# Optimization experiments

Hardware: AMD Instinct MI355X
Metric: run time of the kernel (lower is better)

Reference implementation:

```python
import jax, jax.numpy as jnp
import numpy as np
from jax.ops import segment_sum

N_NODES = 50000


def graph_conv(src, dst, x, W, b, n_nodes):
    # DGL GraphConv with norm='both' (allow_zero_in_degree=True):
    # h = D_in^{-1/2} * A^T (D_out^{-1/2} * x) W + b, degrees clamped to >=1
    ones = jnp.ones(src.shape[0], dtype=x.dtype)
    deg_out = jnp.clip(segment_sum(ones, src, num_segments=n_nodes), 1.0)
    deg_in = jnp.clip(segment_sum(ones, dst, num_segments=n_nodes), 1.0)
    h = x * jax.lax.rsqrt(deg_out)[:, None]
    h = h @ W                      # apply weight before aggregation (mult_W first)
    m = segment_sum(h[src], dst, num_segments=n_nodes)  # sparse neighbor sum
    return m * jax.lax.rsqrt(deg_in)[:, None] + b


def setup_inputs() -> dict:
    key = jax.random.key(0)
    ks = jax.random.split(key, 10)
    n, e = N_NODES, 1600000
    d_in, h1, h2, h3 = 128, 128, 128, 64
    in_feat = jax.random.normal(ks[0], (n, d_in), dtype=jnp.float32)
    src = jax.random.randint(ks[1], (e,), 0, n, dtype=jnp.int32)
    dst = jax.random.randint(ks[2], (e,), 0, n, dtype=jnp.int32)
    s = lambda fi, fo: (1.0 / np.sqrt(fi)).astype(np.float32)
    W1 = jax.random.normal(ks[3], (d_in, h1), dtype=jnp.float32) * s(d_in, h1)
    b1 = jnp.zeros((h1,), dtype=jnp.float32)
    W2 = jax.random.normal(ks[4], (h1, h2), dtype=jnp.float32) * s(h1, h2)
    b2 = jnp.zeros((h2,), dtype=jnp.float32)
    Wf = jax.random.normal(ks[5], (h2, h3), dtype=jnp.float32) * s(h2, h3)
    bf = jnp.zeros((h3,), dtype=jnp.float32)
    return {"in_feat": in_feat, "src": src, "dst": dst,
            "W1": W1, "b1": b1, "W2": W2, "b2": b2, "Wf": Wf, "bf": bf}


def reference(in_feat, src, dst, W1, b1, W2, b2, Wf, bf):
    n = in_feat.shape[0]
    h = graph_conv(src, dst, in_feat, W1, b1, n)
    h = jax.nn.relu(h)
    # dropout(p=0.2) is identity in eval mode
    h = graph_conv(src, dst, h, W2, b2, n)
    return h @ Wf + bf
```

## Files before the change

kernel.cpp:

```cpp
#include <hip/hip_runtime.h>
#include <hip/hip_fp16.h>

#define FD 128
#define OD 64
#define RN 256
#define CHUNKS 256
#define NRMAX 1024

typedef _Float16 f16x8 __attribute__((ext_vector_type(8)));
typedef float    f32x4 __attribute__((ext_vector_type(4)));


__global__ void prescale_kernel(const float* __restrict__ X, const float* __restrict__ r_out,
                                __half* __restrict__ Xs, int n4) {
    int i = blockIdx.x * 256 + threadIdx.x;
    if (i >= n4) return;
    int v = i >> 5;
    float r = r_out[v];
    float4 t = ((const float4*)X)[i];
    __half2 h0 = __floats2half2_rn(t.x * r, t.y * r);
    __half2 h1 = __floats2half2_rn(t.z * r, t.w * r);
    ((__half2*)Xs)[2 * i]     = h0;
    ((__half2*)Xs)[2 * i + 1] = h1;
}


__global__ __launch_bounds__(1024) void region_hist_kernel(const int* __restrict__ src,
                                                           const int* __restrict__ dst,
                                                           int* __restrict__ hist_g,
                                                           int* __restrict__ hist_gs,
                                                           int E, int NR, int CS) {
    __shared__ int hist[NRMAX];
    __shared__ int hist_s[NRMAX];
    int c = blockIdx.x;
    for (int t = threadIdx.x; t < NR; t += 1024) { hist[t] = 0; hist_s[t] = 0; }
    __syncthreads();
    int e0 = c * CS, e1 = min(e0 + CS, E);
    int nv = (e1 - e0) & ~3;
    for (int e = e0 + threadIdx.x * 4; e < e0 + nv; e += 4096) {
        int4 d = *(const int4*)(dst + e);
        int4 s = *(const int4*)(src + e);
        atomicAdd(&hist[d.x >> 8], 1);
        atomicAdd(&hist[d.y >> 8], 1);
        atomicAdd(&hist[d.z >> 8], 1);
        atomicAdd(&hist[d.w >> 8], 1);
        atomicAdd(&hist_s[s.x >> 8], 1);
        atomicAdd(&hist_s[s.y >> 8], 1);
        atomicAdd(&hist_s[s.z >> 8], 1);
        atomicAdd(&hist_s[s.w >> 8], 1);
    }
    for (int e = e0 + nv + threadIdx.x; e < e1; e += 1024) {
        atomicAdd(&hist[dst[e] >> 8], 1);
        atomicAdd(&hist_s[src[e] >> 8], 1);
    }
    __syncthreads();
    for (int t = threadIdx.x; t < NR; t += 1024) {
        hist_g[c * NR + t]  = hist[t];
        hist_gs[c * NR + t] = hist_s[t];
    }
}

__global__ __launch_bounds__(1024) void region_scan_kernel(const int* __restrict__ hist_g,
                                                           const int* __restrict__ hist_gs,
                                                           int* __restrict__ rstart,
                                                           int* __restrict__ cursor,
                                                           int* __restrict__ sstart,
                                                           int* __restrict__ scursor,
                                                           int NR, int E) {
    __shared__ int wsum[16];
    int tid = threadIdx.x, lane = tid & 63, w = tid >> 6;
    int total = 0;
    if (tid < NR)
        for (int c = 0; c < CHUNKS; c++) total += hist_g[c * NR + tid];
    int x = total;
    #pragma unroll
    for (int d = 1; d < 64; d <<= 1) {
        int t = __shfl_up(x, d, 64);
        if (lane >= d) x += t;
    }
    if (lane == 63) wsum[w] = x;
    __syncthreads();
    if (w == 0) {
        int s = (lane < 16) ? wsum[lane] : 0;
        #pragma unroll
        for (int d = 1; d < 16; d <<= 1) {
            int t = __shfl_up(s, d, 64);
            if (lane >= d) s += t;
        }
        if (lane < 16) wsum[lane] = s;
    }
    __syncthreads();
    int off = (w == 0) ? 0 : wsum[w - 1];
    if (tid < NR) {
        int start = x + off - total;
        rstart[tid] = start;
        int run = start;
        for (int c = 0; c < CHUNKS; c++) {
            cursor[c * NR + tid] = run;
            run += hist_g[c * NR + tid];
        }
    }
    if (tid == 0) rstart[NR] = E;
    __syncthreads();
    total = 0;
    if (tid < NR)
        for (int c = 0; c < CHUNKS; c++) total += hist_gs[c * NR + tid];
    x = total;
    #pragma unroll
    for (int d = 1; d < 64; d <<= 1) {
        int t = __shfl_up(x, d, 64);
        if (lane >= d) x += t;
    }
    if (lane == 63) wsum[w] = x;
    __syncthreads();
    if (w == 0) {
        int s = (lane < 16) ? wsum[lane] : 0;
        #pragma unroll
        for (int d = 1; d < 16; d <<= 1) {
            int t = __shfl_up(s, d, 64);
            if (lane >= d) s += t;
        }
        if (lane < 16) wsum[lane] = s;
    }
    __syncthreads();
    off = (w == 0) ? 0 : wsum[w - 1];
    if (tid < NR) {
        int start = x + off - total;
        sstart[tid] = start;
        int run = start;
        for (int c = 0; c < CHUNKS; c++) {
            scursor[c * NR + tid] = run;
            run += hist_gs[c * NR + tid];
        }
    }
    if (tid == 0) sstart[NR] = E;
}

__global__ __launch_bounds__(1024) void partition_kernel(const int* __restrict__ src,
                                                         const int* __restrict__ dst,
                                                         const int* __restrict__ cursor,
                                                         const int* __restrict__ scursor,
                                                         int* __restrict__ epack,
                                                         unsigned char* __restrict__ spack,
                                                         int E, int NR, int CS) {
    __shared__ int cur[NRMAX];
    __shared__ int scur[NRMAX];
    int c = blockIdx.x;
    for (int t = threadIdx.x; t < NR; t += 1024) {
        cur[t]  = cursor[c * NR + t];
        scur[t] = scursor[c * NR + t];
    }
    __syncthreads();
    int e0 = c * CS, e1 = min(e0 + CS, E);
    int nv = (e1 - e0) & ~3;
    for (int e = e0 + threadIdx.x * 4; e < e0 + nv; e += 4096) {
        int4 d = *(const int4*)(dst + e);
        int4 s = *(const int4*)(src + e);
        int p0 = atomicAdd(&cur[d.x >> 8], 1);
        int p1 = atomicAdd(&cur[d.y >> 8], 1);
        int p2 = atomicAdd(&cur[d.z >> 8], 1);
        int p3 = atomicAdd(&cur[d.w >> 8], 1);
        epack[p0] = ((d.x & 255) << 17) | s.x;
        epack[p1] = ((d.y & 255) << 17) | s.y;
        epack[p2] = ((d.z & 255) << 17) | s.z;
        epack[p3] = ((d.w & 255) << 17) | s.w;
        int q0 = atomicAdd(&scur[s.x >> 8], 1);
        int q1 = atomicAdd(&scur[s.y >> 8], 1);
        int q2 = atomicAdd(&scur[s.z >> 8], 1);
        int q3 = atomicAdd(&scur[s.w >> 8], 1);
        spack[q0] = (unsigned char)(s.x & 255);
        spack[q1] = (unsigned char)(s.y & 255);
        spack[q2] = (unsigned char)(s.z & 255);
        spack[q3] = (unsigned char)(s.w & 255);
    }
    for (int e = e0 + nv + threadIdx.x; e < e1; e += 1024) {
        int d = dst[e], s = src[e];
        int pos = atomicAdd(&cur[d >> 8], 1);
        epack[pos] = ((d & 255) << 17) | s;
        int qos = atomicAdd(&scur[s >> 8], 1);
        spack[qos] = (unsigned char)(s & 255);
    }
}

__global__ __launch_bounds__(1024) void region_sort_kernel(const int* __restrict__ epack,
                                                           const int* __restrict__ rstart,
                                                           int* __restrict__ csrc,
                                                           int* __restrict__ row_start,
                                                           float* __restrict__ r_in,
                                                           int N, int NR, int E) {
    __shared__ int cnt[RN];
    __shared__ int cur[RN];
    __shared__ int wsum[16];
    const int r = blockIdx.x, tid = threadIdx.x;
    const int lane = tid & 63, w = tid >> 6;
    const int s0 = rstart[r], s1 = rstart[r + 1];
    if (tid < RN) cnt[tid] = 0;
    __syncthreads();
    for (int e = s0 + tid; e < s1; e += 1024)
        atomicAdd(&cnt[epack[e] >> 17], 1);
    __syncthreads();
    int cv = (tid < RN) ? cnt[tid] : 0;
    int x = cv;
    #pragma unroll
    for (int d = 1; d < 64; d <<= 1) {
        int t = __shfl_up(x, d, 64);
        if (lane >= d) x += t;
    }
    if (lane == 63 && w < 4) wsum[w] = x;
    __syncthreads();
    if (tid < RN) {
        int woff = 0;
        for (int i = 0; i < w; i++) woff += wsum[i];
        int start = s0 + x - cv + woff;
        cur[tid] = start;
        int node = r * RN + tid;
        if (node < N) {
            row_start[node] = start;
            r_in[node] = rsqrtf((float)max(cv, 1));
        }
    }
    if (r == NR - 1 && tid == 0) row_start[N] = E;
    __syncthreads();
    for (int e = s0 + tid; e < s1; e += 1024) {
        int pk = epack[e];
        int pos = atomicAdd(&cur[pk >> 17], 1);
        csrc[pos] = pk & 0x1FFFF;
    }
}

__global__ __launch_bounds__(256) void rout2_kernel(const unsigned char* __restrict__ spack,
                                                    const int* __restrict__ sstart,
                                                    float* __restrict__ r_out, int N) {
    __shared__ int cnt[RN];
    const int r = blockIdx.x, tid = threadIdx.x;
    const int s0 = sstart[r], s1 = sstart[r + 1];
    cnt[tid] = 0;
    __syncthreads();
    for (int e = s0 + tid; e < s1; e += 256)
        atomicAdd(&cnt[spack[e]], 1);
    __syncthreads();
    int node = r * RN + tid;
    if (node < N) r_out[node] = rsqrtf((float)max(cnt[tid], 1));
}

__global__ __launch_bounds__(256) void agg128_kernel(const __half* __restrict__ Xs,
                                                     const float* __restrict__ r_in,
                                                     const int* __restrict__ rs,
                                                     const int* __restrict__ csrc,
                                                     __half* __restrict__ Z, int N) {
    const int lane = threadIdx.x & 63, wv = threadIdx.x >> 6;
    int v = blockIdx.x * 4 + wv;
    if (v >= N) return;
    int s0 = rs[v], s1 = rs[v + 1];
    float ax = 0.f, ay = 0.f;
    int e = s0;
    for (; e + 16 <= s1; e += 16) {
        int idx[16];
        #pragma unroll
        for (int u = 0; u < 16; u++) idx[u] = csrc[e + u];
        __half2 t[16];
        #pragma unroll
        for (int u = 0; u < 16; u++)
            t[u] = ((const __half2*)(Xs + (size_t)idx[u] * FD))[lane];
        #pragma unroll
        for (int u = 0; u < 16; u++) {
            float2 f = __half22float2(t[u]);
            ax += f.x; ay += f.y;
        }
    }
    for (; e + 4 <= s1; e += 4) {
        int idx[4];
        #pragma unroll
        for (int u = 0; u < 4; u++) idx[u] = csrc[e + u];
        __half2 t[4];
        #pragma unroll
        for (int u = 0; u < 4; u++)
            t[u] = ((const __half2*)(Xs + (size_t)idx[u] * FD))[lane];
        #pragma unroll
        for (int u = 0; u < 4; u++) {
            float2 f = __half22float2(t[u]);
            ax += f.x; ay += f.y;
        }
    }
    for (; e < s1; e++) {
        float2 f = __half22float2(((const __half2*)(Xs + (size_t)csrc[e] * FD))[lane]);
        ax += f.x; ay += f.y;
    }
    float ri = r_in[v];
    ((__half2*)(Z + (size_t)v * FD))[lane] = __floats2half2_rn(ax * ri, ay * ri);
}

__global__ __launch_bounds__(256) void agg64_kernel(const __half* __restrict__ T,
                                                    const float* __restrict__ r_in,
                                                    const int* __restrict__ rs,
                                                    const int* __restrict__ csrc,
                                                    const float* __restrict__ bc,
                                                    float* __restrict__ out, int N) {
    const int tid = threadIdx.x;
    const int lane = tid & 63, wv = tid >> 6;
    const int hf = lane >> 5, l32 = lane & 31;
    int v = blockIdx.x * 8 + wv * 2 + hf;
    if (v >= N) return;
    int s0 = rs[v], s1 = rs[v + 1];
    float ax = 0.f, ay = 0.f;
    int e = s0;
    for (; e + 8 <= s1; e += 8) {
        int idx[8];
        #pragma unroll
        for (int u = 0; u < 8; u++) idx[u] = csrc[e + u];
        __half2 t[8];
        #pragma unroll
        for (int u = 0; u < 8; u++)
            t[u] = ((const __half2*)(T + (size_t)idx[u] * OD))[l32];
        #pragma unroll
        for (int u = 0; u < 8; u++) {
            float2 f = __half22float2(t[u]);
            ax += f.x; ay += f.y;
        }
    }
    for (; e < s1; e++) {
        float2 f = __half22float2(((const __half2*)(T + (size_t)csrc[e] * OD))[l32]);
        ax += f.x; ay += f.y;
    }
    float ri = r_in[v];
    float2 o;
    o.x = ax * ri + bc[l32 * 2];
    o.y = ay * ri + bc[l32 * 2 + 1];
    ((float2*)(out + (size_t)v * OD))[l32] = o;
}

__global__ __launch_bounds__(256) void gemm1_mfma_kernel(const __half* __restrict__ Ah,
                                                         const __half* __restrict__ Bh,
                                                         const float* __restrict__ b1,
                                                         const float* __restrict__ rowscale,
                                                         __half* __restrict__ Ch,
                                                         int M, int ntiles) {
    const int w = threadIdx.x >> 6, lane = threadIdx.x & 63;
    const int l15 = lane & 15, quad = lane >> 4;
    const _Float16* B = (const _Float16*)Bh;

    f16x8 bfrag[2][4];
    #pragma unroll
    for (int nt = 0; nt < 2; nt++) {
        int col = 32 * w + 16 * nt + l15;
        #pragma unroll
        for (int kk = 0; kk < 4; kk++) {
            int kb = kk * 32 + quad * 8;
            f16x8 bf;
            #pragma unroll
            for (int j = 0; j < 8; j++) bf[j] = B[(size_t)(kb + j) * FD + col];
            bfrag[nt][kk] = bf;
        }
    }

    for (int t = blockIdx.x; t < ntiles; t += gridDim.x) {
        int row0 = t * 16;
        const _Float16* Arow = (const _Float16*)Ah + (size_t)(row0 + l15) * FD + quad * 8;
        f16x8 afrag[4];
        #pragma unroll
        for (int kk = 0; kk < 4; kk++) afrag[kk] = *(const f16x8*)(Arow + kk * 32);
        f32x4 acc0 = {0.f, 0.f, 0.f, 0.f};
        f32x4 acc1 = {0.f, 0.f, 0.f, 0.f};
        #pragma unroll
        for (int kk = 0; kk < 4; kk++) {
            acc0 = __builtin_amdgcn_mfma_f32_16x16x32_f16(afrag[kk], bfrag[0][kk], acc0, 0, 0, 0);
            acc1 = __builtin_amdgcn_mfma_f32_16x16x32_f16(afrag[kk], bfrag[1][kk], acc1, 0, 0, 0);
        }
        int c0 = 32 * w + l15, c1 = c0 + 16;
        float bb0 = b1[c0], bb1 = b1[c1];
        #pragma unroll
        for (int r = 0; r < 4; r++) {
            int row = row0 + quad * 4 + r;
            if (row < M) {
                float rsc = rowscale[row];
                Ch[(size_t)row * FD + c0] = __float2half(fmaxf(acc0[r] + bb0, 0.f) * rsc);
                Ch[(size_t)row * FD + c1] = __float2half(fmaxf(acc1[r] + bb1, 0.f) * rsc);
            }
        }
    }
}

__global__ __launch_bounds__(256) void gemm2_mfma_kernel(const __half* __restrict__ Ah,
                                                         const __half* __restrict__ Bh,
                                                         __half* __restrict__ Ch,
                                                         int M, int ntiles) {
    const int w = threadIdx.x >> 6, lane = threadIdx.x & 63;
    const int l15 = lane & 15, quad = lane >> 4;
    const _Float16* B = (const _Float16*)Bh;

    f16x8 bfrag[4];
    int col = 16 * w + l15;
    #pragma unroll
    for (int kk = 0; kk < 4; kk++) {
        int kb = kk * 32 + quad * 8;
        f16x8 bf;
        #pragma unroll
        for (int j = 0; j < 8; j++) bf[j] = B[(size_t)(kb + j) * OD + col];
        bfrag[kk] = bf;
    }

    for (int t = blockIdx.x; t < ntiles; t += gridDim.x) {
        int row0 = t * 16;
        const _Float16* Arow = (const _Float16*)Ah + (size_t)(row0 + l15) * FD + quad * 8;
        f16x8 afrag[4];
        #pragma unroll
        for (int kk = 0; kk < 4; kk++) afrag[kk] = *(const f16x8*)(Arow + kk * 32);
        f32x4 acc = {0.f, 0.f, 0.f, 0.f};
        #pragma unroll
        for (int kk = 0; kk < 4; kk++)
            acc = __builtin_amdgcn_mfma_f32_16x16x32_f16(afrag[kk], bfrag[kk], acc, 0, 0, 0);
        #pragma unroll
        for (int r = 0; r < 4; r++) {
            int row = row0 + quad * 4 + r;
            if (row < M)
                Ch[(size_t)row * OD + col] = __float2half(acc[r]);
        }
    }
}

__global__ void fold_kernel(const float* __restrict__ W2, const float* __restrict__ Wf,
                            const float* __restrict__ b2, const float* __restrict__ bf,
                            const float* __restrict__ W1,
                            __half* __restrict__ W1h, __half* __restrict__ Wch,
                            float* __restrict__ bc) {
    int idx = blockIdx.x * 256 + threadIdx.x;
    if (idx < FD * FD) W1h[idx] = __float2half(W1[idx]);
    if (idx < FD * OD) {
        int i = idx / OD, j = idx % OD;
        float s = 0.f;
        for (int k = 0; k < FD; k++) s += W2[i * FD + k] * Wf[k * OD + j];
        Wch[idx] = __float2half(s);
    }
    if (idx < OD) {
        float s = bf[idx];
        for (int k = 0; k < FD; k++) s += b2[k] * Wf[k * OD + idx];
        bc[idx] = s;
    }
}

extern "C" void kernel_launch(void* const* d_in, const int* in_sizes, int n_in,
                              void* d_out, int out_size, void* d_ws, size_t ws_size,
                              hipStream_t stream) {
    const float* in_feat = (const float*)d_in[0];
    const int*   src     = (const int*)d_in[1];
    const int*   dst     = (const int*)d_in[2];
    const float* W1      = (const float*)d_in[3];
    const float* b1      = (const float*)d_in[4];
    const float* W2      = (const float*)d_in[5];
    const float* b2      = (const float*)d_in[6];
    const float* Wf      = (const float*)d_in[7];
    const float* bf      = (const float*)d_in[8];
    float* out = (float*)d_out;

    const int N = in_sizes[0] / FD;
    const int E = in_sizes[1];
    const int NR = (N + RN - 1) / RN;
    const int CS = (((E + CHUNKS - 1) / CHUNKS) + 3) & ~3;

    char* ws = (char*)d_ws;
    size_t off = 0;
    auto alloc = [&](size_t bytes) -> void* {
        void* p = ws + off;
        off += (bytes + 255) / 256 * 256;
        return p;
    };
    unsigned char* spack = (unsigned char*)alloc((size_t)E);
    int*    epack   = (int*)alloc((size_t)E * 4);
    __half* tbuf    = (__half*)spack;
    float*  r_out   = (float*)alloc((size_t)N * 4);
    float*  r_in    = (float*)alloc((size_t)N * 4);
    int*    hist_g  = (int*)alloc((size_t)CHUNKS * NR * 4);
    int*    hist_gs = (int*)alloc((size_t)CHUNKS * NR * 4);
    int*    cursor  = (int*)alloc((size_t)CHUNKS * NR * 4);
    int*    scursor = (int*)alloc((size_t)CHUNKS * NR * 4);
    int*    rstart  = (int*)alloc((size_t)(NR + 1) * 4);
    int*    sstart  = (int*)alloc((size_t)(NR + 1) * 4);
    int*    csrc    = (int*)alloc((size_t)E * 4);
    int*    row_start = (int*)alloc((size_t)(N + 1) * 4);
    __half* z1h     = (__half*)alloc((size_t)N * FD * 2);
    __half* y1h     = (__half*)alloc((size_t)N * FD * 2);
    __half* Xs      = (__half*)alloc((size_t)N * FD * 2);
    __half* W1h     = (__half*)alloc((size_t)FD * FD * 2);
    __half* Wch     = (__half*)alloc((size_t)FD * OD * 2);
    float*  bc      = (float*)alloc((size_t)OD * 4);
    (void)ws_size; (void)n_in; (void)out_size;

    const int ntiles = (N + 15) / 16;
    const int gemmgrid = ntiles < 1024 ? ntiles : 1024;

    region_hist_kernel<<<CHUNKS, 1024, 0, stream>>>(src, dst, hist_g, hist_gs, E, NR, CS);
    region_scan_kernel<<<1, 1024, 0, stream>>>(hist_g, hist_gs, rstart, cursor, sstart, scursor, NR, E);
    partition_kernel<<<CHUNKS, 1024, 0, stream>>>(src, dst, cursor, scursor, epack, spack, E, NR, CS);
    region_sort_kernel<<<NR, 1024, 0, stream>>>(epack, rstart, csrc, row_start, r_in, N, NR, E);
    rout2_kernel<<<NR, 256, 0, stream>>>(spack, sstart, r_out, N);

    fold_kernel<<<(FD * FD + 255) / 256, 256, 0, stream>>>(W2, Wf, b2, bf, W1, W1h, Wch, bc);

    prescale_kernel<<<(N * 32 + 255) / 256, 256, 0, stream>>>(in_feat, r_out, Xs, N * 32);
    agg128_kernel<<<(N + 3) / 4, 256, 0, stream>>>(Xs, r_in, row_start, csrc, z1h, N);

    gemm1_mfma_kernel<<<gemmgrid, 256, 0, stream>>>(z1h, W1h, b1, r_out, y1h, N, ntiles);
    gemm2_mfma_kernel<<<gemmgrid, 256, 0, stream>>>(y1h, Wch, tbuf, N, ntiles);

    agg64_kernel<<<(N + 7) / 8, 256, 0, stream>>>(tbuf, r_in, row_start, csrc, bc, out, N);
}
```

Before: 282.3 us.

## Chunk feature dimension into 32-wide slabs for cache-resident neighbor gathers

Stores the prescaled features, the aggregated features and the second-layer transform in a feature-chunked layout: 32 halfs (64 bytes) per node per chunk. Aggregation then runs once per chunk, so each pass gathers from a much smaller table that can stay in L2. Each wave handles one node, with its four 16-lane quads taking different edges, and the partial sums are combined with shuffles. Both GEMMs are adapted to read and write the chunked layout. The cost is reading the edge index list several times, extra kernel launches, and vector index loads that may not be aligned.

After: 390.0 us. 38.1% more time.

```diff
diff --git a/kernel.cpp b/kernel.cpp
--- a/kernel.cpp
+++ b/kernel.cpp
@@ -6,22 +6,27 @@
 #define RN 256
 #define CHUNKS 256
 #define NRMAX 1024
+#define FC 32
 
 typedef _Float16 f16x8 __attribute__((ext_vector_type(8)));
 typedef float    f32x4 __attribute__((ext_vector_type(4)));
 
 
 __global__ void prescale_kernel(const float* __restrict__ X, const float* __restrict__ r_out,
-                                __half* __restrict__ Xs, int n4) {
+                                __half* __restrict__ Xs, int n4, int N) {
     int i = blockIdx.x * 256 + threadIdx.x;
     if (i >= n4) return;
     int v = i >> 5;
+    int fq = i & 31;
     float r = r_out[v];
     float4 t = ((const float4*)X)[i];
     __half2 h0 = __floats2half2_rn(t.x * r, t.y * r);
     __half2 h1 = __floats2half2_rn(t.z * r, t.w * r);
-    ((__half2*)Xs)[2 * i]     = h0;
-    ((__half2*)Xs)[2 * i + 1] = h1;
+    int c  = fq >> 3;
+    int w0 = (fq & 7) * 4;
+    __half2* p = (__half2*)(Xs + ((size_t)c * N + v) * FC + w0);
+    p[0] = h0;
+    p[1] = h1;
 }
 
 
@@ -243,90 +248,108 @@
     if (node < N) r_out[node] = rsqrtf((float)max(cnt[tid], 1));
 }
 
-__global__ __launch_bounds__(256) void agg128_kernel(const __half* __restrict__ Xs,
+__global__ __launch_bounds__(256) void agg32h_kernel(const __half* __restrict__ T,
                                                      const float* __restrict__ r_in,
                                                      const int* __restrict__ rs,
                                                      const int* __restrict__ csrc,
                                                      __half* __restrict__ Z, int N) {
     const int lane = threadIdx.x & 63, wv = threadIdx.x >> 6;
+    const int quad = lane >> 4, l15 = lane & 15;
     int v = blockIdx.x * 4 + wv;
     if (v >= N) return;
-    int s0 = rs[v], s1 = rs[v + 1];
+    int s0 = __builtin_amdgcn_readfirstlane(rs[v]);
+    int s1 = __builtin_amdgcn_readfirstlane(rs[v + 1]);
     float ax = 0.f, ay = 0.f;
     int e = s0;
-    for (; e + 16 <= s1; e += 16) {
-        int idx[16];
-        #pragma unroll
-        for (int u = 0; u < 16; u++) idx[u] = csrc[e + u];
-        __half2 t[16];
-        #pragma unroll
-        for (int u = 0; u < 16; u++)
-            t[u] = ((const __half2*)(Xs + (size_t)idx[u] * FD))[lane];
-        #pragma unroll
-        for (int u = 0; u < 16; u++) {
-            float2 f = __half22float2(t[u]);
-            ax += f.x; ay += f.y;
-        }
-    }
-    for (; e + 4 <= s1; e += 4) {
-        int idx[4];
-        #pragma unroll
-        for (int u = 0; u < 4; u++) idx[u] = csrc[e + u];
-        __half2 t[4];
-        #pragma unroll
-        for (int u = 0; u < 4; u++)
-            t[u] = ((const __half2*)(Xs + (size_t)idx[u] * FD))[lane];
-        #pragma unroll
-        for (int u = 0; u < 4; u++) {
-            float2 f = __half22float2(t[u]);
-            ax += f.x; ay += f.y;
-        }
-    }
-    for (; e < s1; e++) {
-        float2 f = __half22float2(((const __half2*)(Xs + (size_t)csrc[e] * FD))[lane]);
-        ax += f.x; ay += f.y;
-    }
-    float ri = r_in[v];
-    ((__half2*)(Z + (size_t)v * FD))[lane] = __floats2half2_rn(ax * ri, ay * ri);
-}
-
-__global__ __launch_bounds__(256) void agg64_kernel(const __half* __restrict__ T,
-                                                    const float* __restrict__ r_in,
-                                                    const int* __restrict__ rs,
-                                                    const int* __restrict__ csrc,
-                                                    const float* __restrict__ bc,
-                                                    float* __restrict__ out, int N) {
-    const int tid = threadIdx.x;
-    const int lane = tid & 63, wv = tid >> 6;
-    const int hf = lane >> 5, l32 = lane & 31;
-    int v = blockIdx.x * 8 + wv * 2 + hf;
-    if (v >= N) return;
-    int s0 = rs[v], s1 = rs[v + 1];
-    float ax = 0.f, ay = 0.f;
-    int e = s0;
-    for (; e + 8 <= s1; e += 8) {
+    for (; e + 32 <= s1; e += 32) {
         int idx[8];
         #pragma unroll
-        for (int u = 0; u < 8; u++) idx[u] = csrc[e + u];
+        for (int u = 0; u < 8; u++) {
+            int4 q4 = *(const int4*)(csrc + e + 4 * u);
+            idx[u] = quad == 0 ? q4.x : quad == 1 ? q4.y : quad == 2 ? q4.z : q4.w;
+        }
         __half2 t[8];
         #pragma unroll
         for (int u = 0; u < 8; u++)
-            t[u] = ((const __half2*)(T + (size_t)idx[u] * OD))[l32];
+            t[u] = ((const __half2*)(T + (size_t)idx[u] * FC))[l15];
         #pragma unroll
         for (int u = 0; u < 8; u++) {
             float2 f = __half22float2(t[u]);
             ax += f.x; ay += f.y;
         }
     }
+    for (; e + 4 <= s1; e += 4) {
+        int4 q4 = *(const int4*)(csrc + e);
+        int idx = quad == 0 ? q4.x : quad == 1 ? q4.y : quad == 2 ? q4.z : q4.w;
+        float2 f = __half22float2(((const __half2*)(T + (size_t)idx * FC))[l15]);
+        ax += f.x; ay += f.y;
+    }
     for (; e < s1; e++) {
-        float2 f = __half22float2(((const __half2*)(T + (size_t)csrc[e] * OD))[l32]);
+        if (quad == 0) {
+            float2 f = __half22float2(((const __half2*)(T + (size_t)csrc[e] * FC))[l15]);
+            ax += f.x; ay += f.y;
+        }
+    }
+    ax += __shfl_xor(ax, 16); ay += __shfl_xor(ay, 16);
+    ax += __shfl_xor(ax, 32); ay += __shfl_xor(ay, 32);
+    if (quad == 0) {
+        float ri = r_in[v];
+        ((__half2*)(Z + (size_t)v * FC))[l15] = __floats2half2_rn(ax * ri, ay * ri);
+    }
+}
+
+__global__ __launch_bounds__(256) void agg32f_kernel(const __half* __restrict__ T,
+                                                     const float* __restrict__ r_in,
+                                                     const int* __restrict__ rs,
+                                                     const int* __restrict__ csrc,
+                                                     const float* __restrict__ bcc,
+                                                     float* __restrict__ outc, int N) {
+    const int lane = threadIdx.x & 63, wv = threadIdx.x >> 6;
+    const int quad = lane >> 4, l15 = lane & 15;
+    int v = blockIdx.x * 4 + wv;
+    if (v >= N) return;
+    int s0 = __builtin_amdgcn_readfirstlane(rs[v]);
+    int s1 = __builtin_amdgcn_readfirstlane(rs[v + 1]);
+    float ax = 0.f, ay = 0.f;
+    int e = s0;
+    for (; e + 32 <= s1; e += 32) {
+        int idx[8];
+        #pragma unroll
+        for (int u = 0; u < 8; u++) {
+            int4 q4 = *(const int4*)(csrc + e + 4 * u);
+            idx[u] = quad == 0 ? q4.x : quad == 1 ? q4.y : quad == 2 ? q4.z : q4.w;
+        }
+        __half2 t[8];
+        #pragma unroll
+        for (int u = 0; u < 8; u++)
+            t[u] = ((const __half2*)(T + (size_t)idx[u] * FC))[l15];
+        #pragma unroll
+        for (int u = 0; u < 8; u++) {
+            float2 f = __half22float2(t[u]);
+            ax += f.x; ay += f.y;
+        }
+    }
+    for (; e + 4 <= s1; e += 4) {
+        int4 q4 = *(const int4*)(csrc + e);
+        int idx = quad == 0 ? q4.x : quad == 1 ? q4.y : quad == 2 ? q4.z : q4.w;
+        float2 f = __half22float2(((const __half2*)(T + (size_t)idx * FC))[l15]);
         ax += f.x; ay += f.y;
     }
-    float ri = r_in[v];
-    float2 o;
-    o.x = ax * ri + bc[l32 * 2];
-    o.y = ay * ri + bc[l32 * 2 + 1];
-    ((float2*)(out + (size_t)v * OD))[l32] = o;
+    for (; e < s1; e++) {
+        if (quad == 0) {
+            float2 f = __half22float2(((const __half2*)(T + (size_t)csrc[e] * FC))[l15]);
+            ax += f.x; ay += f.y;
+        }
+    }
+    ax += __shfl_xor(ax, 16); ay += __shfl_xor(ay, 16);
+    ax += __shfl_xor(ax, 32); ay += __shfl_xor(ay, 32);
+    if (quad == 0) {
+        float ri = r_in[v];
+        float2 o;
+        o.x = ax * ri + bcc[2 * l15];
+        o.y = ay * ri + bcc[2 * l15 + 1];
+        ((float2*)(outc + (size_t)v * OD))[l15] = o;
+    }
 }
 
 __global__ __launch_bounds__(256) void gemm1_mfma_kernel(const __half* __restrict__ Ah,
@@ -338,6 +361,7 @@
     const int w = threadIdx.x >> 6, lane = threadIdx.x & 63;
     const int l15 = lane & 15, quad = lane >> 4;
     const _Float16* B = (const _Float16*)Bh;
+    const _Float16* Az = (const _Float16*)Ah;
 
     f16x8 bfrag[2][4];
     #pragma unroll
@@ -355,10 +379,10 @@
 
     for (int t = blockIdx.x; t < ntiles; t += gridDim.x) {
         int row0 = t * 16;
-        const _Float16* Arow = (const _Float16*)Ah + (size_t)(row0 + l15) * FD + quad * 8;
         f16x8 afrag[4];
         #pragma unroll
-        for (int kk = 0; kk < 4; kk++) afrag[kk] = *(const f16x8*)(Arow + kk * 32);
+        for (int kk = 0; kk < 4; kk++)
+            afrag[kk] = *(const f16x8*)(Az + ((size_t)kk * M + row0 + l15) * FC + quad * 8);
         f32x4 acc0 = {0.f, 0.f, 0.f, 0.f};
         f32x4 acc1 = {0.f, 0.f, 0.f, 0.f};
         #pragma unroll
@@ -390,6 +414,7 @@
 
     f16x8 bfrag[4];
     int col = 16 * w + l15;
+    const int cc = col >> 5, cw = col & 31;
     #pragma unroll
     for (int kk = 0; kk < 4; kk++) {
         int kb = kk * 32 + quad * 8;
@@ -413,7 +438,7 @@
         for (int r = 0; r < 4; r++) {
             int row = row0 + quad * 4 + r;
             if (row < M)
-                Ch[(size_t)row * OD + col] = __float2half(acc[r]);
+                Ch[((size_t)cc * M + row) * FC + cw] = __float2half(acc[r]);
         }
     }
 }
@@ -496,11 +521,15 @@
 
     fold_kernel<<<(FD * FD + 255) / 256, 256, 0, stream>>>(W2, Wf, b2, bf, W1, W1h, Wch, bc);
 
-    prescale_kernel<<<(N * 32 + 255) / 256, 256, 0, stream>>>(in_feat, r_out, Xs, N * 32);
-    agg128_kernel<<<(N + 3) / 4, 256, 0, stream>>>(Xs, r_in, row_start, csrc, z1h, N);
+    prescale_kernel<<<(N * 32 + 255) / 256, 256, 0, stream>>>(in_feat, r_out, Xs, N * 32, N);
+    for (int c = 0; c < 4; c++)
+        agg32h_kernel<<<(N + 3) / 4, 256, 0, stream>>>(Xs + (size_t)c * N * FC, r_in, row_start,
+                                                       csrc, z1h + (size_t)c * N * FC, N);
 
     gemm1_mfma_kernel<<<gemmgrid, 256, 0, stream>>>(z1h, W1h, b1, r_out, y1h, N, ntiles);
     gemm2_mfma_kernel<<<gemmgrid, 256, 0, stream>>>(y1h, Wch, tbuf, N, ntiles);
 
-    agg64_kernel<<<(N + 7) / 8, 256, 0, stream>>>(tbuf, r_in, row_start, csrc, bc, out, N);
-}
+    for (int c = 0; c < 2; c++)
+        agg32f_kernel<<<(N + 3) / 4, 256, 0, stream>>>(tbuf + (size_t)c * N * FC, r_in, row_start,
+                                                       csrc, bc + c * FC, out + c * FC, N);
+}
```

## Transpose histogram layout and software-pipeline index loads in aggregation kernels

Applied to the files above, without the earlier changes.

The per-chunk region histograms and cursors are stored region-major instead of chunk-major. This lets the single-block scan kernel read and write each region's 256 counts with int4 vector accesses instead of strided scalar ones. The gather-aggregation kernels now prefetch the next block of edge indices while the current block's feature rows are loaded, and replace the scalar tail loops with one masked, clamped batch. They also use nontemporal loads and stores for indices and outputs. The cost is more complex code, some wasted loads in the tail, and larger workspace allocations sized by NRMAX.

After: 287.0 us. Within noise of the previous version (+1.7%).

```diff
diff --git a/kernel.cpp b/kernel.cpp
--- a/kernel.cpp
+++ b/kernel.cpp
@@ -9,6 +9,7 @@
 
 typedef _Float16 f16x8 __attribute__((ext_vector_type(8)));
 typedef float    f32x4 __attribute__((ext_vector_type(4)));
+typedef float    f32x2 __attribute__((ext_vector_type(2)));
 
 
 __global__ void prescale_kernel(const float* __restrict__ X, const float* __restrict__ r_out,
@@ -18,10 +19,8 @@
     int v = i >> 5;
     float r = r_out[v];
     float4 t = ((const float4*)X)[i];
-    __half2 h0 = __floats2half2_rn(t.x * r, t.y * r);
-    __half2 h1 = __floats2half2_rn(t.z * r, t.w * r);
-    ((__half2*)Xs)[2 * i]     = h0;
-    ((__half2*)Xs)[2 * i + 1] = h1;
+    ((__half2*)Xs)[2 * i]     = __floats2half2_rn(t.x * r, t.y * r);
+    ((__half2*)Xs)[2 * i + 1] = __floats2half2_rn(t.z * r, t.w * r);
 }
 
 
@@ -55,8 +54,8 @@
     }
     __syncthreads();
     for (int t = threadIdx.x; t < NR; t += 1024) {
-        hist_g[c * NR + t]  = hist[t];
-        hist_gs[c * NR + t] = hist_s[t];
+        hist_g[t * CHUNKS + c]  = hist[t];
+        hist_gs[t * CHUNKS + c] = hist_s[t];
     }
 }
 
@@ -70,8 +69,14 @@
     __shared__ int wsum[16];
     int tid = threadIdx.x, lane = tid & 63, w = tid >> 6;
     int total = 0;
-    if (tid < NR)
-        for (int c = 0; c < CHUNKS; c++) total += hist_g[c * NR + tid];
+    if (tid < NR) {
+        const int4* hp = (const int4*)(hist_g + (size_t)tid * CHUNKS);
+        #pragma unroll 8
+        for (int c4 = 0; c4 < CHUNKS / 4; c4++) {
+            int4 h = hp[c4];
+            total += h.x + h.y + h.z + h.w;
+        }
+    }
     int x = total;
     #pragma unroll
     for (int d = 1; d < 64; d <<= 1) {
@@ -95,16 +100,30 @@
         int start = x + off - total;
         rstart[tid] = start;
         int run = start;
-        for (int c = 0; c < CHUNKS; c++) {
-            cursor[c * NR + tid] = run;
-            run += hist_g[c * NR + tid];
+        const int4* hp = (const int4*)(hist_g + (size_t)tid * CHUNKS);
+        int4* cp = (int4*)(cursor + (size_t)tid * CHUNKS);
+        #pragma unroll 8
+        for (int c4 = 0; c4 < CHUNKS / 4; c4++) {
+            int4 h = hp[c4];
+            int4 o;
+            o.x = run; run += h.x;
+            o.y = run; run += h.y;
+            o.z = run; run += h.z;
+            o.w = run; run += h.w;
+            cp[c4] = o;
         }
     }
     if (tid == 0) rstart[NR] = E;
     __syncthreads();
     total = 0;
-    if (tid < NR)
-        for (int c = 0; c < CHUNKS; c++) total += hist_gs[c * NR + tid];
+    if (tid < NR) {
+        const int4* hp = (const int4*)(hist_gs + (size_t)tid * CHUNKS);
+        #pragma unroll 8
+        for (int c4 = 0; c4 < CHUNKS / 4; c4++) {
+            int4 h = hp[c4];
+            total += h.x + h.y + h.z + h.w;
+        }
+    }
     x = total;
     #pragma unroll
     for (int d = 1; d < 64; d <<= 1) {
@@ -128,9 +147,17 @@
         int start = x + off - total;
         sstart[tid] = start;
         int run = start;
-        for (int c = 0; c < CHUNKS; c++) {
-            scursor[c * NR + tid] = run;
-            run += hist_gs[c * NR + tid];
+        const int4* hp = (const int4*)(hist_gs + (size_t)tid * CHUNKS);
+        int4* cp = (int4*)(scursor + (size_t)tid * CHUNKS);
+        #pragma unroll 8
+        for (int c4 = 0; c4 < CHUNKS / 4; c4++) {
+            int4 h = hp[c4];
+            int4 o;
+            o.x = run; run += h.x;
+            o.y = run; run += h.y;
+            o.z = run; run += h.z;
+            o.w = run; run += h.w;
+            cp[c4] = o;
         }
     }
     if (tid == 0) sstart[NR] = E;
@@ -147,8 +174,8 @@
     __shared__ int scur[NRMAX];
     int c = blockIdx.x;
     for (int t = threadIdx.x; t < NR; t += 1024) {
-        cur[t]  = cursor[c * NR + t];
-        scur[t] = scursor[c * NR + t];
+        cur[t]  = cursor[(size_t)t * CHUNKS + c];
+        scur[t] = scursor[(size_t)t * CHUNKS + c];
     }
     __syncthreads();
     int e0 = c * CS, e1 = min(e0 + CS, E);
@@ -251,43 +278,61 @@
     const int lane = threadIdx.x & 63, wv = threadIdx.x >> 6;
     int v = blockIdx.x * 4 + wv;
     if (v >= N) return;
-    int s0 = rs[v], s1 = rs[v + 1];
+    int s0 = __builtin_amdgcn_readfirstlane(rs[v]);
+    int s1 = __builtin_amdgcn_readfirstlane(rs[v + 1]);
+    const int deg = s1 - s0;
     float ax = 0.f, ay = 0.f;
+    const int nb = deg >> 4;
     int e = s0;
-    for (; e + 16 <= s1; e += 16) {
-        int idx[16];
-        #pragma unroll
-        for (int u = 0; u < 16; u++) idx[u] = csrc[e + u];
+    if (nb) {
+        int ia[16];
+        #pragma unroll
+        for (int u = 0; u < 16; u++) ia[u] = __builtin_nontemporal_load(csrc + e + u);
+        for (int b = 1; b < nb; b++) {
+            __half2 t[16];
+            #pragma unroll
+            for (int u = 0; u < 16; u++)
+                t[u] = ((const __half2*)(Xs + (size_t)ia[u] * FD))[lane];
+            int eb = e + (b << 4);
+            #pragma unroll
+            for (int u = 0; u < 16; u++) ia[u] = __builtin_nontemporal_load(csrc + eb + u);
+            #pragma unroll
+            for (int u = 0; u < 16; u++) {
+                float2 f = __half22float2(t[u]);
+                ax += f.x; ay += f.y;
+            }
+        }
         __half2 t[16];
         #pragma unroll
         for (int u = 0; u < 16; u++)
-            t[u] = ((const __half2*)(Xs + (size_t)idx[u] * FD))[lane];
+            t[u] = ((const __half2*)(Xs + (size_t)ia[u] * FD))[lane];
         #pragma unroll
         for (int u = 0; u < 16; u++) {
             float2 f = __half22float2(t[u]);
             ax += f.x; ay += f.y;
         }
-    }
-    for (; e + 4 <= s1; e += 4) {
-        int idx[4];
-        #pragma unroll
-        for (int u = 0; u < 4; u++) idx[u] = csrc[e + u];
-        __half2 t[4];
-        #pragma unroll
-        for (int u = 0; u < 4; u++)
-            t[u] = ((const __half2*)(Xs + (size_t)idx[u] * FD))[lane];
-        #pragma unroll
-        for (int u = 0; u < 4; u++) {
-            float2 f = __half22float2(t[u]);
+        e += nb << 4;
+    }
+    const int rem = s1 - e;
+    if (rem) {
+        const int last = s1 - 1;
+        int ia[16];
+        #pragma unroll
+        for (int u = 0; u < 16; u++)
+            ia[u] = __builtin_nontemporal_load(csrc + min(e + u, last));
+        #pragma unroll
+        for (int u = 0; u < 16; u++) {
+            unsigned raw = ((const unsigned*)(Xs + (size_t)ia[u] * FD))[lane];
+            raw = (u < rem) ? raw : 0u;
+            union { unsigned q; __half2 h; } tt; tt.q = raw;
+            float2 f = __half22float2(tt.h);
             ax += f.x; ay += f.y;
         }
     }
-    for (; e < s1; e++) {
-        float2 f = __half22float2(((const __half2*)(Xs + (size_t)csrc[e] * FD))[lane]);
-        ax += f.x; ay += f.y;
-    }
     float ri = r_in[v];
-    ((__half2*)(Z + (size_t)v * FD))[lane] = __floats2half2_rn(ax * ri, ay * ri);
+    union { __half2 h; unsigned q; } o;
+    o.h = __floats2half2_rn(ax * ri, ay * ri);
+    __builtin_nontemporal_store(o.q, (unsigned*)(Z + (size_t)v * FD) + lane);
 }
 
 __global__ __launch_bounds__(256) void agg64_kernel(const __half* __restrict__ T,
@@ -302,31 +347,60 @@
     int v = blockIdx.x * 8 + wv * 2 + hf;
     if (v >= N) return;
     int s0 = rs[v], s1 = rs[v + 1];
+    const int deg = s1 - s0;
     float ax = 0.f, ay = 0.f;
+    const int nb = deg >> 3;
     int e = s0;
-    for (; e + 8 <= s1; e += 8) {
-        int idx[8];
-        #pragma unroll
-        for (int u = 0; u < 8; u++) idx[u] = csrc[e + u];
+    if (nb) {
+        int ia[8];
+        #pragma unroll
+        for (int u = 0; u < 8; u++) ia[u] = __builtin_nontemporal_load(csrc + e + u);
+        for (int b = 1; b < nb; b++) {
+            __half2 t[8];
+            #pragma unroll
+            for (int u = 0; u < 8; u++)
+                t[u] = ((const __half2*)(T + (size_t)ia[u] * OD))[l32];
+            int eb = e + (b << 3);
+            #pragma unroll
+            for (int u = 0; u < 8; u++) ia[u] = __builtin_nontemporal_load(csrc + eb + u);
+            #pragma unroll
+            for (int u = 0; u < 8; u++) {
+                float2 f = __half22float2(t[u]);
+                ax += f.x; ay += f.y;
+            }
+        }
         __half2 t[8];
         #pragma unroll
         for (int u = 0; u < 8; u++)
-            t[u] = ((const __half2*)(T + (size_t)idx[u] * OD))[l32];
+            t[u] = ((const __half2*)(T + (size_t)ia[u] * OD))[l32];
         #pragma unroll
         for (int u = 0; u < 8; u++) {
             float2 f = __half22float2(t[u]);
             ax += f.x; ay += f.y;
         }
-    }
-    for (; e < s1; e++) {
-        float2 f = __half22float2(((const __half2*)(T + (size_t)csrc[e] * OD))[l32]);
-        ax += f.x; ay += f.y;
+        e += nb << 3;
+    }
+    const int rem = s1 - e;
+    if (rem) {
+        const int last = s1 - 1;
+        int ia[8];
+        #pragma unroll
+        for (int u = 0; u < 8; u++)
+            ia[u] = __builtin_nontemporal_load(csrc + min(e + u, last));
+        #pragma unroll
+        for (int u = 0; u < 8; u++) {
+            unsigned raw = ((const unsigned*)(T + (size_t)ia[u] * OD))[l32];
+            raw = (u < rem) ? raw : 0u;
+            union { unsigned q; __half2 h; } tt; tt.q = raw;
+            float2 f = __half22float2(tt.h);
+            ax += f.x; ay += f.y;
+        }
     }
     float ri = r_in[v];
-    float2 o;
+    f32x2 o;
     o.x = ax * ri + bc[l32 * 2];
     o.y = ay * ri + bc[l32 * 2 + 1];
-    ((float2*)(out + (size_t)v * OD))[l32] = o;
+    __builtin_nontemporal_store(o, (f32x2*)(out + (size_t)v * OD) + l32);
 }
 
 __global__ __launch_bounds__(256) void gemm1_mfma_kernel(const __half* __restrict__ Ah,
@@ -469,10 +543,10 @@
     __half* tbuf    = (__half*)spack;
     float*  r_out   = (float*)alloc((size_t)N * 4);
     float*  r_in    = (float*)alloc((size_t)N * 4);
-    int*    hist_g  = (int*)alloc((size_t)CHUNKS * NR * 4);
-    int*    hist_gs = (int*)alloc((size_t)CHUNKS * NR * 4);
-    int*    cursor  = (int*)alloc((size_t)CHUNKS * NR * 4);
-    int*    scursor = (int*)alloc((size_t)CHUNKS * NR * 4);
+    int*    hist_g  = (int*)alloc((size_t)CHUNKS * NRMAX * 4);
+    int*    hist_gs = (int*)alloc((size_t)CHUNKS * NRMAX * 4);
+    int*    cursor  = (int*)alloc((size_t)CHUNKS * NRMAX * 4);
+    int*    scursor = (int*)alloc((size_t)CHUNKS * NRMAX * 4);
     int*    rstart  = (int*)alloc((size_t)(NR + 1) * 4);
     int*    sstart  = (int*)alloc((size_t)(NR + 1) * 4);
     int*    csrc    = (int*)alloc((size_t)E * 4);
```
